# Kernel optimization log

Hardware: AMD Instinct MI355X
Metric: run time of the kernel (lower is better)

The kernel has to match this reference:

```python
import jax, jax.numpy as jnp
import numpy as np

B, C, H, W = 2, 72, 96, 96
FACTOR = 4  # input_dim // output_dim = 72 // 18


def setup_inputs() -> dict:
    key = jax.random.key(0)
    ks = jax.random.split(key, 7)
    s = 1.0 / np.sqrt(C)
    return {
        "x": jax.random.normal(ks[0], (B, C, H, W), dtype=jnp.float32),
        "Wq": jax.random.normal(ks[1], (C, C), dtype=jnp.float32) * s,
        "bq": jax.random.normal(ks[2], (C,), dtype=jnp.float32) * 0.01,
        "Wk": jax.random.normal(ks[3], (C, C), dtype=jnp.float32) * s,
        "bk": jax.random.normal(ks[4], (C,), dtype=jnp.float32) * 0.01,
        "Wv": jax.random.normal(ks[5], (C, C), dtype=jnp.float32) * s,
        "bv": jax.random.normal(ks[6], (C,), dtype=jnp.float32) * 0.01,
    }


def reference(x, Wq, bq, Wk, bk, Wv, bv):
    b, c, h, w = x.shape
    n = h * w
    flat = x.reshape(b, c, n)  # [B, C, N]
    # 1x1 convs == per-pixel channel matmuls
    q = jnp.einsum('dc,bcn->bdn', Wq, flat) + bq[None, :, None]
    k = jnp.einsum('dc,bcn->bdn', Wk, flat) + bk[None, :, None]
    v = jnp.einsum('dc,bcn->bdn', Wv, flat) + bv[None, :, None]
    # scores[b,i,j] = sum_c q[b,c,i] * k[b,c,j]  (no 1/sqrt(d) scaling, as in source)
    scores = jnp.einsum('bci,bcj->bij', q, k)  # [B, N, N]
    attn = jax.nn.softmax(scores, axis=-1)
    # weighted_values = bmm(v, attn^T): wv[b,c,i] = sum_j v[b,c,j] * attn[b,i,j]
    wv = jnp.einsum('bcj,bij->bci', v, attn)  # [B, C, N]
    wv = wv.reshape(b, c // FACTOR, FACTOR, h, w)
    xg = x.reshape(b, c // FACTOR, FACTOR, h, w)
    pooled = jnp.sum(xg * wv, axis=2)  # [B, C//FACTOR, H, W]
    return pooled
```

## Files before the change

### kernel.cpp

```cpp
#include <hip/hip_runtime.h>

#define NPIX 9216
#define CIN 72
#define CP 96
#define SPLITS 8
#define JCHUNK (NPIX / SPLITS)
#define JTILES (JCHUNK / 64)
#define L2E   1.44269504088896f
#define EXPB  46.1662413084468f

typedef __attribute__((ext_vector_type(8))) short bf16x8;
typedef __attribute__((ext_vector_type(8))) _Float16 f16x8;
typedef __attribute__((ext_vector_type(4))) float f32x4;

#define MFMA_BF16(A,B,C) __builtin_amdgcn_mfma_f32_16x16x32_bf16(A,B,C,0,0,0)
#define MFMA_F16(A,B,C)  __builtin_amdgcn_mfma_f32_16x16x32_f16(A,B,C,0,0,0)

static __device__ __forceinline__ unsigned short f2bf(float f) {
  unsigned u = __float_as_uint(f);
  u += 0x7fffu + ((u >> 16) & 1u);
  return (unsigned short)(u >> 16);
}
static __device__ __forceinline__ float bf2f(unsigned short h) {
  return __uint_as_float(((unsigned)h) << 16);
}
static __device__ __forceinline__ unsigned short f2h(float f) {
  _Float16 h = (_Float16)f;
  return *(unsigned short*)&h;
}
static __device__ __forceinline__ unsigned pack_bf_trunc(float lo, float hi) {
  return (__float_as_uint(lo) >> 16) | (__float_as_uint(hi) & 0xffff0000u);
}
static __device__ __forceinline__ void load_lds16(const void* g, void* l) {
  __builtin_amdgcn_global_load_lds(
      (const __attribute__((address_space(1))) unsigned int*)g,
      (__attribute__((address_space(3))) unsigned int*)l, 16, 0, 0);
}

__global__ __launch_bounds__(256) void wprep_kernel(
    const float* __restrict__ Wq, const float* __restrict__ Wk,
    const float* __restrict__ Wv,
    unsigned short* __restrict__ WH, unsigned short* __restrict__ WL)
{
  int id = blockIdx.x * 256 + threadIdx.x;
  if (id >= 3 * 80 * 96) return;
  int mat = id / (80 * 96);
  int rem = id % (80 * 96);
  int d = rem / 96, c = rem % 96;
  const float* W = (mat == 0) ? Wq : (mat == 1) ? Wk : Wv;
  float v = (d < 72 && c < 72) ? W[d * 72 + c] : 0.f;
  unsigned short hi = f2bf(v);
  WH[id] = hi;
  WL[id] = f2bf(v - bf2f(hi));
}

#define XTS 104

__global__ __launch_bounds__(256) void qkv_kernel(
    const float* __restrict__ x,
    const unsigned short* __restrict__ WH, const unsigned short* __restrict__ WL,
    const float* __restrict__ bq, const float* __restrict__ bk,
    const float* __restrict__ bv,
    unsigned short* __restrict__ QH, unsigned short* __restrict__ KH,
    unsigned short* __restrict__ VG)
{
  __shared__ __align__(16) unsigned short obuf[4][16 * XTS];

  const int t    = threadIdx.x;
  const int ww   = t >> 6;
  const int lane = t & 63;
  const int quad = lane >> 4;
  const int l15  = lane & 15;

  const int task  = blockIdx.x * 4 + ww;
  const int m     = task % 3;
  const int strip = task / 3;
  const int b     = strip / 576;
  const int n0    = (strip % 576) * 16;

  bf16x8 xbh[3], xbl[3];
#pragma unroll
  for (int ks = 0; ks < 3; ++ks) {
#pragma unroll
    for (int j = 0; j < 8; ++j) {
      int c = ks * 32 + quad * 8 + j;
      c = (c < 72) ? c : 71;
      float v = x[((size_t)b * CIN + c) * NPIX + n0 + l15];
      unsigned short hi = f2bf(v);
      ((unsigned short*)&xbh[ks])[j] = hi;
      ((unsigned short*)&xbl[ks])[j] = f2bf(v - bf2f(hi));
    }
  }

  const unsigned short* wh = WH + m * 80 * 96;
  const unsigned short* wl = WL + m * 80 * 96;
  const float* bias = (m == 0) ? bq : (m == 1) ? bk : bv;

  f32x4 acc[5];
#pragma unroll
  for (int dm = 0; dm < 5; ++dm) {
    acc[dm] = (f32x4){0.f, 0.f, 0.f, 0.f};
#pragma unroll
    for (int ks = 0; ks < 3; ++ks) {
      bf16x8 ah = *(const bf16x8*)(wh + (dm * 16 + l15) * 96 + ks * 32 + quad * 8);
      bf16x8 al = *(const bf16x8*)(wl + (dm * 16 + l15) * 96 + ks * 32 + quad * 8);
      acc[dm] = MFMA_BF16(ah, xbh[ks], acc[dm]);
      acc[dm] = MFMA_BF16(ah, xbl[ks], acc[dm]);
      acc[dm] = MFMA_BF16(al, xbh[ks], acc[dm]);
    }
  }

  if (m < 2) {
    unsigned short* ob = obuf[ww];
#pragma unroll
    for (int dm = 0; dm < 5; ++dm)
#pragma unroll
      for (int r = 0; r < 4; ++r) {
        int d = dm * 16 + quad * 4 + r;
        float v = acc[dm][r] + (d < 72 ? bias[d] : 0.f);
        ob[l15 * XTS + d] = f2h(v);
      }
    unsigned short* outp = (m == 0) ? QH : KH;
    const size_t obase = ((size_t)b * NPIX + n0) * CP;
    uint4 z; z.x = z.y = z.z = z.w = 0u;
    for (int f = lane; f < 192; f += 64) {
      int row = f / 12, col = f % 12;
      *(uint4*)(outp + obase + (size_t)row * CP + col * 8) =
          (col < 10) ? *(const uint4*)(ob + row * XTS + col * 8) : z;
    }
  } else {
#pragma unroll
    for (int dm = 0; dm < 5; ++dm)
#pragma unroll
      for (int r = 0; r < 4; ++r) {
        int d = dm * 16 + quad * 4 + r;
        float v = (d < 72) ? acc[dm][r] + bias[d] : (d == 72 ? 1.0f : 0.f);
        VG[((size_t)b * 80 + d) * NPIX + n0 + l15] = f2bf(v);
      }
  }
}

#define KCH 12
#define VCH 10

__global__ __launch_bounds__(256, 3) void flash_kernel(
    const float* __restrict__ x,
    const unsigned short* __restrict__ QH, const unsigned short* __restrict__ KH,
    const unsigned short* __restrict__ VG,
    float* __restrict__ NUM, float* __restrict__ LPART)
{
  __shared__ __align__(16) unsigned short ls_kh[KCH * 512];
  __shared__ __align__(16) unsigned short ls_vs[VCH * 512];

  const int t    = threadIdx.x;
  const int w    = t >> 6;
  const int lane = t & 63;
  const int quad = lane >> 4;
  const int l15  = lane & 15;

  const int bid  = blockIdx.x;
  const int sp   = bid & 7;
  const int slot = bid >> 3;
  const int b    = slot / 48;
  const int it   = slot % 48;
  const int i0w  = it * 192 + w * 48;

  f16x8 qh[3][3];
#pragma unroll
  for (int mi = 0; mi < 3; ++mi)
#pragma unroll
    for (int ks = 0; ks < 3; ++ks) {
      size_t off = ((size_t)b * NPIX + i0w + mi * 16 + l15) * CP + ks * 32 + quad * 8;
      qh[mi][ks] = *(const f16x8*)(QH + off);
    }

  f32x4 oacc[3][5];
#pragma unroll
  for (int mi = 0; mi < 3; ++mi)
#pragma unroll
    for (int nt = 0; nt < 5; ++nt) oacc[mi][nt] = (f32x4){0.f, 0.f, 0.f, 0.f};

  const unsigned short* kpg = KH + ((size_t)b * NPIX + sp * JCHUNK) * CP;
  const unsigned short* vpg = VG + (size_t)b * 80 * NPIX + sp * JCHUNK;

  int koff[3], voff[3];
#pragma unroll
  for (int k = 0; k < 3; ++k) {
    int c = w + 4 * k;
    koff[k] = ((c / 3) * 16 + l15) * CP + (c % 3) * 32 + quad * 8;
    int cv = (c < VCH) ? c : 0;
    voff[k] = ((cv >> 1) * 16 + l15) * NPIX + (cv & 1) * 32 + quad * 8;
  }

  for (int jt = 0; jt < JTILES; ++jt, kpg += 64 * CP, vpg += 64) {
#pragma unroll
    for (int k = 0; k < 3; ++k)
      load_lds16(kpg + koff[k], ls_kh + (w + 4 * k) * 512);
#pragma unroll
    for (int k = 0; k < 3; ++k)
      if (w + 4 * k < VCH)
        load_lds16(vpg + voff[k], ls_vs + (w + 4 * k) * 512);
    __syncthreads();

#pragma unroll
    for (int js = 0; js < 2; ++js) {
      uint2 pkA[3], pkB[3];
#pragma unroll
      for (int tjh = 0; tjh < 2; ++tjh) {
        const int tj = js * 2 + tjh;
        f16x8 fkh[3];
#pragma unroll
        for (int ks = 0; ks < 3; ++ks)
          fkh[ks] = *(const f16x8*)(ls_kh + (tj * 3 + ks) * 512 + lane * 8);
#pragma unroll
        for (int mi = 0; mi < 3; ++mi) {
          f32x4 s = (f32x4){0.f, 0.f, 0.f, 0.f};
          s = MFMA_F16(fkh[0], qh[mi][0], s);
          s = MFMA_F16(fkh[1], qh[mi][1], s);
          s = MFMA_F16(fkh[2], qh[mi][2], s);
          float p0 = __builtin_amdgcn_exp2f(__builtin_fmaf(s[0], L2E, -EXPB));
          float p1 = __builtin_amdgcn_exp2f(__builtin_fmaf(s[1], L2E, -EXPB));
          float p2 = __builtin_amdgcn_exp2f(__builtin_fmaf(s[2], L2E, -EXPB));
          float p3 = __builtin_amdgcn_exp2f(__builtin_fmaf(s[3], L2E, -EXPB));
          uint2 pk;
          pk.x = pack_bf_trunc(p0, p1);
          pk.y = pack_bf_trunc(p2, p3);
          if (tjh == 0) pkA[mi] = pk; else pkB[mi] = pk;
        }
      }

      bf16x8 pf[3];
#pragma unroll
      for (int mi = 0; mi < 3; ++mi) {
        unsigned x0 = pkA[mi].x, x1 = pkB[mi].x;
        asm("v_permlane32_swap_b32 %0, %1" : "+v"(x0), "+v"(x1));
        asm("v_permlane16_swap_b32 %0, %1" : "+v"(x0), "+v"(x1));
        unsigned y0 = pkA[mi].y, y1 = pkB[mi].y;
        asm("v_permlane32_swap_b32 %0, %1" : "+v"(y0), "+v"(y1));
        asm("v_permlane16_swap_b32 %0, %1" : "+v"(y0), "+v"(y1));
        uint4 fr;
        fr.x = x0; fr.y = y0; fr.z = x1; fr.w = y1;
        pf[mi] = *(const bf16x8*)&fr;
      }

#pragma unroll
      for (int nt = 0; nt < 5; ++nt) {
        bf16x8 vf = *(const bf16x8*)(ls_vs + (nt * 2 + js) * 512 + lane * 8);
#pragma unroll
        for (int mi = 0; mi < 3; ++mi)
          oacc[mi][nt] = MFMA_BF16(vf, pf[mi], oacc[mi][nt]);
      }
    }
    __syncthreads();
  }

  const size_t sb = (size_t)(sp * 2 + b);
#pragma unroll
  for (int mi = 0; mi < 3; ++mi) {
    const int i = i0w + mi * 16 + l15;
    if (quad == 2)
      LPART[sb * NPIX + i] = oacc[mi][4][0];
#pragma unroll
    for (int nt = 0; nt < 5; ++nt) {
      int c0 = nt * 16 + quad * 4;
      if (c0 < 72) {
        float num = 0.f;
#pragma unroll
        for (int r = 0; r < 4; ++r)
          num = __builtin_fmaf(x[((size_t)b * CIN + c0 + r) * NPIX + i],
                               oacc[mi][nt][r], num);
        NUM[(sb * 18 + (c0 >> 2)) * NPIX + i] = num;
      }
    }
  }
}

__global__ __launch_bounds__(256) void combine_pool_kernel(
    const float* __restrict__ NUM, const float* __restrict__ LPART,
    float* __restrict__ out)
{
  int id = blockIdx.x * 256 + threadIdx.x;
  if (id >= 2 * 18 * (NPIX / 4)) return;
  int n = (id % (NPIX / 4)) * 4;
  int rest = id / (NPIX / 4);
  int g = rest % 18, b = rest / 18;

  float4 A = make_float4(0.f, 0.f, 0.f, 0.f);
  float4 L = make_float4(0.f, 0.f, 0.f, 0.f);
#pragma unroll
  for (int s = 0; s < SPLITS; ++s) {
    size_t sb = (size_t)(s * 2 + b);
    float4 a = *(const float4*)(NUM + (sb * 18 + g) * NPIX + n);
    float4 l = *(const float4*)(LPART + sb * NPIX + n);
    A.x += a.x; A.y += a.y; A.z += a.z; A.w += a.w;
    L.x += l.x; L.y += l.y; L.z += l.z; L.w += l.w;
  }
  float4 r;
  r.x = A.x / L.x; r.y = A.y / L.y; r.z = A.z / L.z; r.w = A.w / L.w;
  *(float4*)(out + (size_t)id * 4) = r;
}

extern "C" void kernel_launch(void* const* d_in, const int* in_sizes, int n_in,
                              void* d_out, int out_size, void* d_ws, size_t ws_size,
                              hipStream_t stream) {
  const float* x  = (const float*)d_in[0];
  const float* Wq = (const float*)d_in[1];
  const float* bq = (const float*)d_in[2];
  const float* Wk = (const float*)d_in[3];
  const float* bk = (const float*)d_in[4];
  const float* Wv = (const float*)d_in[5];
  const float* bv = (const float*)d_in[6];
  float* out = (float*)d_out;

  char* p = (char*)d_ws;
  const size_t szQK = (size_t)2 * NPIX * CP * 2;
  unsigned short* QH = (unsigned short*)p; p += szQK;
  unsigned short* KH = (unsigned short*)p; p += szQK;
  unsigned short* VG = (unsigned short*)p; p += (size_t)2 * 80 * NPIX * 2;
  unsigned short* WH = (unsigned short*)p; p += (size_t)3 * 80 * 96 * 2;
  unsigned short* WL = (unsigned short*)p; p += (size_t)3 * 80 * 96 * 2;
  float* NUM = (float*)p; p += (size_t)SPLITS * 2 * 18 * NPIX * 4;
  float* LPART = (float*)p; p += (size_t)SPLITS * 2 * NPIX * 4;

  wprep_kernel<<<(3 * 80 * 96 + 255) / 256, 256, 0, stream>>>(Wq, Wk, Wv, WH, WL);
  qkv_kernel<<<864, 256, 0, stream>>>(x, WH, WL, bq, bk, bv, QH, KH, VG);
  flash_kernel<<<SPLITS * 2 * 48, 256, 0, stream>>>(x, QH, KH, VG, NUM, LPART);
  combine_pool_kernel<<<(2 * 18 * (NPIX / 4) + 255) / 256, 256, 0, stream>>>(
      NUM, LPART, out);
}
```

Measured before the change: 153.3 us.

## Fuse weight prep into QKV and combine into flash via grid barrier

Removes the separate weight-splitting kernel by converting the fp32 weights to bf16 hi/lo pairs inline inside the QKV kernel. It also removes the combine/pool kernel: the flash kernel now ends with a global atomic-counter barrier, after which its blocks perform the split reduction and normalization. This cuts two kernel launches and their gaps. The cost is redundant weight conversion per wave and a spin-wait grid barrier that relies on all 768 flash blocks being co-resident, which risks deadlock if occupancy is insufficient.

```diff
diff --git a/kernel.cpp b/kernel.cpp
--- a/kernel.cpp
+++ b/kernel.cpp
@@ -6,6 +6,7 @@
 #define SPLITS 8
 #define JCHUNK (NPIX / SPLITS)
 #define JTILES (JCHUNK / 64)
+#define FGRID (SPLITS * 2 * 48)
 #define L2E   1.44269504088896f
 #define EXPB  46.1662413084468f
 
@@ -37,32 +38,16 @@
       (__attribute__((address_space(3))) unsigned int*)l, 16, 0, 0);
 }
 
-__global__ __launch_bounds__(256) void wprep_kernel(
+#define XTS 104
+
+__global__ __launch_bounds__(256) void qkv_kernel(
+    const float* __restrict__ x,
     const float* __restrict__ Wq, const float* __restrict__ Wk,
     const float* __restrict__ Wv,
-    unsigned short* __restrict__ WH, unsigned short* __restrict__ WL)
-{
-  int id = blockIdx.x * 256 + threadIdx.x;
-  if (id >= 3 * 80 * 96) return;
-  int mat = id / (80 * 96);
-  int rem = id % (80 * 96);
-  int d = rem / 96, c = rem % 96;
-  const float* W = (mat == 0) ? Wq : (mat == 1) ? Wk : Wv;
-  float v = (d < 72 && c < 72) ? W[d * 72 + c] : 0.f;
-  unsigned short hi = f2bf(v);
-  WH[id] = hi;
-  WL[id] = f2bf(v - bf2f(hi));
-}
-
-#define XTS 104
-
-__global__ __launch_bounds__(256) void qkv_kernel(
-    const float* __restrict__ x,
-    const unsigned short* __restrict__ WH, const unsigned short* __restrict__ WL,
     const float* __restrict__ bq, const float* __restrict__ bk,
     const float* __restrict__ bv,
     unsigned short* __restrict__ QH, unsigned short* __restrict__ KH,
-    unsigned short* __restrict__ VG)
+    unsigned short* __restrict__ VG, unsigned* done)
 {
   __shared__ __align__(16) unsigned short obuf[4][16 * XTS];
 
@@ -71,6 +56,9 @@
   const int lane = t & 63;
   const int quad = lane >> 4;
   const int l15  = lane & 15;
+
+  if (blockIdx.x == 0 && t == 0)
+    __hip_atomic_store(done, 0u, __ATOMIC_RELAXED, __HIP_MEMORY_SCOPE_AGENT);
 
   const int task  = blockIdx.x * 4 + ww;
   const int m     = task % 3;
@@ -92,18 +80,29 @@
     }
   }
 
-  const unsigned short* wh = WH + m * 80 * 96;
-  const unsigned short* wl = WL + m * 80 * 96;
+  const float* Wm   = (m == 0) ? Wq : (m == 1) ? Wk : Wv;
   const float* bias = (m == 0) ? bq : (m == 1) ? bk : bv;
 
   f32x4 acc[5];
 #pragma unroll
   for (int dm = 0; dm < 5; ++dm) {
     acc[dm] = (f32x4){0.f, 0.f, 0.f, 0.f};
+    const int d = dm * 16 + l15;
 #pragma unroll
     for (int ks = 0; ks < 3; ++ks) {
-      bf16x8 ah = *(const bf16x8*)(wh + (dm * 16 + l15) * 96 + ks * 32 + quad * 8);
-      bf16x8 al = *(const bf16x8*)(wl + (dm * 16 + l15) * 96 + ks * 32 + quad * 8);
+      const int c0 = ks * 32 + quad * 8;
+      bf16x8 ah = (bf16x8)(short)0, al = (bf16x8)(short)0;
+      if (d < 72 && c0 < 72) {
+        float4 wa = *(const float4*)(Wm + d * 72 + c0);
+        float4 wb = *(const float4*)(Wm + d * 72 + c0 + 4);
+        float wv[8] = {wa.x, wa.y, wa.z, wa.w, wb.x, wb.y, wb.z, wb.w};
+#pragma unroll
+        for (int j = 0; j < 8; ++j) {
+          unsigned short hi = f2bf(wv[j]);
+          ((unsigned short*)&ah)[j] = hi;
+          ((unsigned short*)&al)[j] = f2bf(wv[j] - bf2f(hi));
+        }
+      }
       acc[dm] = MFMA_BF16(ah, xbh[ks], acc[dm]);
       acc[dm] = MFMA_BF16(ah, xbl[ks], acc[dm]);
       acc[dm] = MFMA_BF16(al, xbh[ks], acc[dm]);
@@ -147,7 +146,8 @@
     const float* __restrict__ x,
     const unsigned short* __restrict__ QH, const unsigned short* __restrict__ KH,
     const unsigned short* __restrict__ VG,
-    float* __restrict__ NUM, float* __restrict__ LPART)
+    float* __restrict__ NUM, float* __restrict__ LPART,
+    float* __restrict__ out, unsigned* done)
 {
   __shared__ __align__(16) unsigned short ls_kh[KCH * 512];
   __shared__ __align__(16) unsigned short ls_vs[VCH * 512];
@@ -273,31 +273,39 @@
       }
     }
   }
-}
-
-__global__ __launch_bounds__(256) void combine_pool_kernel(
-    const float* __restrict__ NUM, const float* __restrict__ LPART,
-    float* __restrict__ out)
-{
-  int id = blockIdx.x * 256 + threadIdx.x;
-  if (id >= 2 * 18 * (NPIX / 4)) return;
-  int n = (id % (NPIX / 4)) * 4;
-  int rest = id / (NPIX / 4);
-  int g = rest % 18, b = rest / 18;
-
-  float4 A = make_float4(0.f, 0.f, 0.f, 0.f);
-  float4 L = make_float4(0.f, 0.f, 0.f, 0.f);
-#pragma unroll
-  for (int s = 0; s < SPLITS; ++s) {
-    size_t sb = (size_t)(s * 2 + b);
-    float4 a = *(const float4*)(NUM + (sb * 18 + g) * NPIX + n);
-    float4 l = *(const float4*)(LPART + sb * NPIX + n);
-    A.x += a.x; A.y += a.y; A.z += a.z; A.w += a.w;
-    L.x += l.x; L.y += l.y; L.z += l.z; L.w += l.w;
-  }
-  float4 r;
-  r.x = A.x / L.x; r.y = A.y / L.y; r.z = A.z / L.z; r.w = A.w / L.w;
-  *(float4*)(out + (size_t)id * 4) = r;
+
+  __threadfence();
+  __syncthreads();
+  if (t == 0) {
+    __hip_atomic_fetch_add(done, 1u, __ATOMIC_RELEASE, __HIP_MEMORY_SCOPE_AGENT);
+    unsigned v;
+    do {
+      __builtin_amdgcn_s_sleep(8);
+      v = __hip_atomic_load(done, __ATOMIC_ACQUIRE, __HIP_MEMORY_SCOPE_AGENT);
+    } while (v < FGRID);
+  }
+  __syncthreads();
+  __threadfence();
+
+  int cid = bid * 256 + t;
+  if (cid < 2 * 18 * (NPIX / 4)) {
+    int n = (cid % (NPIX / 4)) * 4;
+    int rest = cid / (NPIX / 4);
+    int g = rest % 18, cb = rest / 18;
+    float4 A = make_float4(0.f, 0.f, 0.f, 0.f);
+    float4 L = make_float4(0.f, 0.f, 0.f, 0.f);
+#pragma unroll
+    for (int s = 0; s < SPLITS; ++s) {
+      size_t sb2 = (size_t)(s * 2 + cb);
+      float4 a = *(const float4*)(NUM + (sb2 * 18 + g) * NPIX + n);
+      float4 l = *(const float4*)(LPART + sb2 * NPIX + n);
+      A.x += a.x; A.y += a.y; A.z += a.z; A.w += a.w;
+      L.x += l.x; L.y += l.y; L.z += l.z; L.w += l.w;
+    }
+    float4 r;
+    r.x = A.x / L.x; r.y = A.y / L.y; r.z = A.z / L.z; r.w = A.w / L.w;
+    *(float4*)(out + (size_t)cid * 4) = r;
+  }
 }
 
 extern "C" void kernel_launch(void* const* d_in, const int* in_sizes, int n_in,
@@ -317,14 +325,10 @@
   unsigned short* QH = (unsigned short*)p; p += szQK;
   unsigned short* KH = (unsigned short*)p; p += szQK;
   unsigned short* VG = (unsigned short*)p; p += (size_t)2 * 80 * NPIX * 2;
-  unsigned short* WH = (unsigned short*)p; p += (size_t)3 * 80 * 96 * 2;
-  unsigned short* WL = (unsigned short*)p; p += (size_t)3 * 80 * 96 * 2;
   float* NUM = (float*)p; p += (size_t)SPLITS * 2 * 18 * NPIX * 4;
   float* LPART = (float*)p; p += (size_t)SPLITS * 2 * NPIX * 4;
-
-  wprep_kernel<<<(3 * 80 * 96 + 255) / 256, 256, 0, stream>>>(Wq, Wk, Wv, WH, WL);
-  qkv_kernel<<<864, 256, 0, stream>>>(x, WH, WL, bq, bk, bv, QH, KH, VG);
-  flash_kernel<<<SPLITS * 2 * 48, 256, 0, stream>>>(x, QH, KH, VG, NUM, LPART);
-  combine_pool_kernel<<<(2 * 18 * (NPIX / 4) + 255) / 256, 256, 0, stream>>>(
-      NUM, LPART, out);
-}
+  unsigned* done = (unsigned*)p; p += 64;
+
+  qkv_kernel<<<864, 256, 0, stream>>>(x, Wq, Wk, Wv, bq, bk, bv, QH, KH, VG, done);
+  flash_kernel<<<FGRID, 256, 0, stream>>>(x, QH, KH, VG, NUM, LPART, out, done);
+}
```

Measured after the change: 391.7 us. +155.5%, slower.
